# Performance work log

Hardware: AMD Instinct MI355X
Metric: run time of the kernel (lower is better)

## Reference

```python
import jax, jax.numpy as jnp
import numpy as np

B, S, D, H, F, R = 4, 128, 512, 8, 2048, 8
DH = D // H
THRESH = 0.1  # hardcoded in the torch module


def _ln(x, g, b):
    m = x.mean(-1, keepdims=True)
    v = ((x - m) ** 2).mean(-1, keepdims=True)
    return (x - m) * jax.lax.rsqrt(v + 1e-5) * g + b


def setup_inputs() -> dict:
    key = jax.random.key(0)
    ks = jax.random.split(key, 12)
    w = lambda k, shape, std: jax.random.normal(k, shape, jnp.float32) * std
    s = 1.0 / np.sqrt(D)
    qk_std = 2.0 / np.sqrt(D)  # peaky attention so adjacency threshold fires
    return {
        "x": jax.random.normal(ks[0], (B, S, D), jnp.float32),
        "ln1_g": jnp.ones(D, jnp.float32), "ln1_b": jnp.zeros(D, jnp.float32),
        "wq": w(ks[1], (D, D), qk_std), "bq": jnp.zeros(D, jnp.float32),
        "wk": w(ks[2], (D, D), qk_std), "bk": jnp.zeros(D, jnp.float32),
        "wv": w(ks[3], (D, D), s), "bv": jnp.zeros(D, jnp.float32),
        "wo": w(ks[4], (D, D), s), "bo": jnp.zeros(D, jnp.float32),
        "w1": w(ks[5], (D, F), s), "b1": jnp.zeros(F, jnp.float32),
        "w2": w(ks[6], (F, D), 1.0 / np.sqrt(F)), "b2": jnp.zeros(D, jnp.float32),
        "rc_w1": w(ks[7], (2 * D, D), 1.0 / np.sqrt(2 * D)), "rc_b1": jnp.zeros(D, jnp.float32),
        "rc_w2": w(ks[8], (D, R), s), "rc_b2": jnp.zeros(R, jnp.float32),
        "kg_w": w(ks[9], (R, D, D), s),
        "s2n_w": w(ks[10], (D, D), s), "s2n_b": jnp.zeros(D, jnp.float32),
        "ln2_g": jnp.ones(D, jnp.float32), "ln2_b": jnp.zeros(D, jnp.float32),
    }


def reference(x, ln1_g, ln1_b, wq, bq, wk, bk, wv, bv, wo, bo,
              w1, b1, w2, b2, rc_w1, rc_b1, rc_w2, rc_b2,
              kg_w, s2n_w, s2n_b, ln2_g, ln2_b):
    # pre-norm attention
    xn = _ln(x, ln1_g, ln1_b)
    q = (xn @ wq + bq).reshape(B, S, H, DH)
    k = (xn @ wk + bk).reshape(B, S, H, DH)
    v = (xn @ wv + bv).reshape(B, S, H, DH)
    scores = jnp.einsum('bihd,bjhd->bhij', q, k) / np.sqrt(DH)
    attn = jax.nn.softmax(scores, axis=-1)                  # [B,H,S,S]
    ctx = jnp.einsum('bhij,bjhd->bihd', attn, v).reshape(B, S, D)
    attn_out = ctx @ wo + bo
    # FFN -> neural_understanding (no residual, as in source)
    nu = jax.nn.relu(attn_out @ w1 + b1) @ w2 + b2          # [B,S,D]
    # dynamic edge extraction, expressed as a dense mask (jit-safe)
    am = attn.mean(axis=1)                                  # [B,S,S]
    adj = (am > THRESH) & (~jnp.eye(S, dtype=bool))         # u != v
    # relation classifier on every (u,v) pair; mask selects real edges
    a_part = nu @ rc_w1[:D]                                 # concept1 half
    b_part = nu @ rc_w1[D:]                                 # concept2 half
    h = jax.nn.relu(a_part[:, :, None, :] + b_part[:, None, :, :] + rc_b1)  # [B,S,S,D]
    logits = h @ rc_w2 + rc_b2                              # [B,S,S,R]
    pred = jnp.argmax(logits, axis=-1)
    valid = adj & (pred != 0)                               # relation 0 == NONE
    oh = jax.nn.one_hot(pred, R, dtype=nu.dtype) * valid[..., None].astype(nu.dtype)
    # RGCN-style knowledge graph conv: message u -> v with per-relation weight
    transformed = jnp.einsum('bud,rde->bure', nu, kg_w)     # [B,S,R,D]
    agg = jnp.einsum('buvr,bure->bve', oh, transformed)     # [B,S,D]
    reasoned = nu + agg
    neural_result = reasoned @ s2n_w + s2n_b
    out = _ln(x + neural_result, ln2_g, ln2_b)
    return out
```

## Files before the change

kernel.cpp:

```cpp
#include <hip/hip_runtime.h>
#include <hip/hip_bf16.h>

#define B_ 4
#define S_ 128
#define D_ 512
#define H_ 8
#define DH_ 64
#define F_ 2048
#define R_ 8
#define BS_ (B_ * S_)
#define BSD_ (BS_ * D_)
#define E_ 262144

typedef __attribute__((ext_vector_type(8))) short short8;
typedef __attribute__((ext_vector_type(4))) float f32x4;
typedef __attribute__((ext_vector_type(4))) unsigned short ushort4v;

__device__ __forceinline__ void split2(float a, unsigned short& h, unsigned short& l) {
    unsigned u = __float_as_uint(a);
    unsigned hr = (u + 0x7FFFu + ((u >> 16) & 1u)) >> 16;
    h = (unsigned short)hr;
    float lo = a - __uint_as_float(hr << 16);
    unsigned u2 = __float_as_uint(lo);
    l = (unsigned short)((u2 + 0x7FFFu + ((u2 >> 16) & 1u)) >> 16);
}

struct TDesc { const float* s; unsigned short* h; unsigned short* l; int K; int N; int off; };
struct TPack { TDesc d[10]; };

__global__ void prep_kernel(TPack p, int nt, const float* __restrict__ x,
                            const float* __restrict__ g, const float* __restrict__ be,
                            unsigned short* __restrict__ xh, unsigned short* __restrict__ xl) {
    __shared__ float tr[32][33];
    __shared__ float red[256];
    int bid = blockIdx.x;
    if (bid < nt) {
        int wi = 0;
#pragma unroll
        for (int i = 1; i < 10; ++i) if (bid >= p.d[i].off) wi = i;
        const TDesc dd = p.d[wi];
        int t = bid - dd.off;
        int ntk = dd.K / 32;
        int tk = t % ntk, tn = t / ntk;
        int k0 = tk * 32, n0 = tn * 32;
        int col = threadIdx.x & 31, rg = threadIdx.x >> 5;
#pragma unroll
        for (int i = 0; i < 4; ++i) {
            int row = rg * 4 + i;
            tr[row][col] = dd.s[(size_t)(k0 + row) * dd.N + n0 + col];
        }
        __syncthreads();
#pragma unroll
        for (int i = 0; i < 4; ++i) {
            int n = n0 + rg * 4 + i;
            int k = k0 + col;
            unsigned short h, l;
            split2(tr[col][rg * 4 + i], h, l);
            dd.h[(size_t)n * dd.K + k] = h;
            dd.l[(size_t)n * dd.K + k] = l;
        }
    } else {
        int row = bid - nt;
        int t = threadIdx.x;
        const float* xr = x + (size_t)row * D_;
        float v0 = xr[t], v1 = xr[t + 256];
        red[t] = v0 + v1;
        __syncthreads();
        for (int off = 128; off > 0; off >>= 1) { if (t < off) red[t] += red[t + off]; __syncthreads(); }
        float mean = red[0] * (1.0f / D_);
        __syncthreads();
        float d0 = v0 - mean, d1 = v1 - mean;
        red[t] = d0 * d0 + d1 * d1;
        __syncthreads();
        for (int off = 128; off > 0; off >>= 1) { if (t < off) red[t] += red[t + off]; __syncthreads(); }
        float rs = rsqrtf(red[0] * (1.0f / D_) + 1e-5f);
        float o0 = d0 * rs * g[t] + be[t];
        float o1 = d1 * rs * g[t + 256] + be[t + 256];
        unsigned short h, l;
        split2(o0, h, l); xh[(size_t)row * D_ + t] = h;       xl[(size_t)row * D_ + t] = l;
        split2(o1, h, l); xh[(size_t)row * D_ + t + 256] = h; xl[(size_t)row * D_ + t + 256] = l;
    }
}

struct GemmLds {
    unsigned short A[3][2][64][64];
    unsigned short B[3][2][64][64];
};

__device__ __forceinline__ void gload16(const unsigned short* g, unsigned short* l) {
    __builtin_amdgcn_global_load_lds(
        (const __attribute__((address_space(1))) void*)g,
        (__attribute__((address_space(3))) void*)l, 16, 0, 0);
}

__device__ __forceinline__ void vmwait_batches(int nb) {
    if (nb == 2)      asm volatile("s_waitcnt vmcnt(16)" ::: "memory");
    else if (nb == 1) asm volatile("s_waitcnt vmcnt(8)" ::: "memory");
    else              asm volatile("s_waitcnt vmcnt(0)" ::: "memory");
}

__device__ __forceinline__ void mgemm_core(const unsigned short* __restrict__ Ath,
                                           const unsigned short* __restrict__ Atl,
                                           const unsigned short* __restrict__ Bth,
                                           const unsigned short* __restrict__ Btl,
                                           int K, int rowBase, int colBase,
                                           int kStart, int nsteps,
                                           f32x4 acc[2][2], GemmLds* L) {
    int tid = threadIdx.x;
    int w = tid >> 6, lane = tid & 63;
    int lm = lane & 15, quad = lane >> 4;
    int wm = (w & 1) * 32, wn = (w >> 1) * 32;
    int r0 = w * 8 + (lane >> 3);
    int lc = ((lane & 7) ^ (lane >> 3)) * 8;
    int wb = w * 512;
    size_t a0 = (size_t)(rowBase + r0) * K + kStart + lc;
    size_t a1 = (size_t)(rowBase + r0 + 32) * K + kStart + lc;
    size_t b0 = (size_t)(colBase + r0) * K + kStart + lc;
    size_t b1 = (size_t)(colBase + r0 + 32) * K + kStart + lc;
    unsigned short* AB = &L->A[0][0][0][0];
    unsigned short* BB = &L->B[0][0][0][0];
    auto stage = [&](int buf, size_t koff) {
        gload16(&Ath[a0 + koff], AB + buf * 8192 + wb);
        gload16(&Ath[a1 + koff], AB + buf * 8192 + 2048 + wb);
        gload16(&Atl[a0 + koff], AB + buf * 8192 + 4096 + wb);
        gload16(&Atl[a1 + koff], AB + buf * 8192 + 6144 + wb);
        gload16(&Bth[b0 + koff], BB + buf * 8192 + wb);
        gload16(&Bth[b1 + koff], BB + buf * 8192 + 2048 + wb);
        gload16(&Btl[b0 + koff], BB + buf * 8192 + 4096 + wb);
        gload16(&Btl[b1 + koff], BB + buf * 8192 + 6144 + wb);
    };
    stage(0, 0);
    if (nsteps > 1) stage(1, 64);
    if (nsteps > 2) stage(2, 128);
    int b = 0;
    for (int s = 0; s < nsteps; ++s) {
        int last = nsteps - 1;
        int inflight = (s + 2 <= last) ? 2 : (s + 1 <= last) ? 1 : 0;
        vmwait_batches(inflight);
        __builtin_amdgcn_s_barrier();
        __builtin_amdgcn_sched_barrier(0);
#pragma unroll
        for (int sub = 0; sub < 2; ++sub) {
            short8 ah[2], al[2], bh[2], bl[2];
            int pc = ((sub * 4 + quad) ^ (lm & 7)) * 8;
#pragma unroll
            for (int t = 0; t < 2; ++t) {
                int ra = (wm + t * 16 + lm) * 64 + pc;
                int rb = (wn + t * 16 + lm) * 64 + pc;
                ah[t] = *(const short8*)(AB + b * 8192 + ra);
                al[t] = *(const short8*)(AB + b * 8192 + 4096 + ra);
                bh[t] = *(const short8*)(BB + b * 8192 + rb);
                bl[t] = *(const short8*)(BB + b * 8192 + 4096 + rb);
            }
#pragma unroll
            for (int tm = 0; tm < 2; ++tm)
#pragma unroll
                for (int tn = 0; tn < 2; ++tn) {
                    acc[tm][tn] = __builtin_amdgcn_mfma_f32_16x16x32_bf16(ah[tm], bh[tn], acc[tm][tn], 0, 0, 0);
                    acc[tm][tn] = __builtin_amdgcn_mfma_f32_16x16x32_bf16(ah[tm], bl[tn], acc[tm][tn], 0, 0, 0);
                    acc[tm][tn] = __builtin_amdgcn_mfma_f32_16x16x32_bf16(al[tm], bh[tn], acc[tm][tn], 0, 0, 0);
                }
        }
        __builtin_amdgcn_sched_barrier(0);
        __builtin_amdgcn_s_barrier();
        if (s + 3 < nsteps) stage(b, (size_t)(s + 3) * 64);
        b = (b == 2) ? 0 : b + 1;
    }
}

__device__ __forceinline__ void gemm_epilogue(f32x4 acc[2][2], const float* bias,
                                              float* Cf, unsigned short* Ch, unsigned short* Cl,
                                              int N, int relu, int rowBase, int colBase) {
    int tid = threadIdx.x;
    int w = tid >> 6, lane = tid & 63;
    int lm = lane & 15, quad = lane >> 4;
    int wm = (w & 1) * 32, wn = (w >> 1) * 32;
#pragma unroll
    for (int tm = 0; tm < 2; ++tm)
#pragma unroll
        for (int tn = 0; tn < 2; ++tn) {
            int col = colBase + wn + tn * 16 + lm;
            float bi = bias ? bias[col] : 0.f;
#pragma unroll
            for (int r = 0; r < 4; ++r) {
                int row = rowBase + wm + tm * 16 + quad * 4 + r;
                float v = acc[tm][tn][r] + bi;
                if (relu) v = fmaxf(v, 0.f);
                size_t o = (size_t)row * N + col;
                if (Cf) Cf[o] = v;
                if (Ch) {
                    unsigned short sh, sl;
                    split2(v, sh, sl);
                    Ch[o] = sh; Cl[o] = sl;
                }
            }
        }
}

__global__ __launch_bounds__(256) void mgemm_kernel(const unsigned short* __restrict__ Ath,
                                                    const unsigned short* __restrict__ Atl,
                                                    const unsigned short* __restrict__ Bth,
                                                    const unsigned short* __restrict__ Btl,
                                                    const float* __restrict__ bias,
                                                    float* __restrict__ Cf,
                                                    unsigned short* __restrict__ Ch,
                                                    unsigned short* __restrict__ Cl,
                                                    int N, int K, int relu) {
    __shared__ GemmLds L;
    int rowBase = blockIdx.y * 64, colBase = blockIdx.x * 64;
    f32x4 acc[2][2] = {};
    mgemm_core(Ath, Atl, Bth, Btl, K, rowBase, colBase, 0, K / 64, acc, &L);
    gemm_epilogue(acc, bias, Cf, Ch, Cl, N, relu, rowBase, colBase);
}

__global__ __launch_bounds__(256) void mgemm_zw_kernel(const unsigned short* __restrict__ Ath,
                                                       const unsigned short* __restrict__ Atl,
                                                       const unsigned short* __restrict__ Bth,
                                                       const unsigned short* __restrict__ Btl,
                                                       const float* __restrict__ b0,
                                                       const float* __restrict__ b1,
                                                       const float* __restrict__ b2,
                                                       float* __restrict__ Cbase,
                                                       int M, int N, int K) {
    __shared__ GemmLds L;
    int z = blockIdx.z;
    const unsigned short* bth = Bth + (size_t)z * K * N;
    const unsigned short* btl = Btl + (size_t)z * K * N;
    const float* bias = (z == 0) ? b0 : (z == 1) ? b1 : b2;
    float* C = Cbase + (size_t)z * M * N;
    int rowBase = blockIdx.y * 64, colBase = blockIdx.x * 64;
    f32x4 acc[2][2] = {};
    mgemm_core(Ath, Atl, bth, btl, K, rowBase, colBase, 0, K / 64, acc, &L);
    gemm_epilogue(acc, bias, C, nullptr, nullptr, N, 0, rowBase, colBase);
}

__global__ __launch_bounds__(256) void mgemm_part_kernel(const unsigned short* __restrict__ Ath,
                                                         const unsigned short* __restrict__ Atl,
                                                         const unsigned short* __restrict__ Bth,
                                                         const unsigned short* __restrict__ Btl,
                                                         float* __restrict__ Cbase,
                                                         int M, int N, int K) {
    __shared__ GemmLds L;
    int ks = gridDim.z, z = blockIdx.z;
    int kLen = K / ks, kStart = z * kLen;
    float* C = Cbase + (size_t)z * M * N;
    int rowBase = blockIdx.y * 64, colBase = blockIdx.x * 64;
    f32x4 acc[2][2] = {};
    mgemm_core(Ath, Atl, Bth, Btl, K, rowBase, colBase, kStart, kLen / 64, acc, &L);
    gemm_epilogue(acc, nullptr, C, nullptr, nullptr, N, 0, rowBase, colBase);
}

__global__ __launch_bounds__(256) void wo_adj_kernel(const unsigned short* __restrict__ Ath,
                                                     const unsigned short* __restrict__ Atl,
                                                     const unsigned short* __restrict__ Bth,
                                                     const unsigned short* __restrict__ Btl,
                                                     const float* __restrict__ bias,
                                                     unsigned short* __restrict__ Ch,
                                                     unsigned short* __restrict__ Cl,
                                                     const float* __restrict__ attnP,
                                                     unsigned long long* __restrict__ adjm) {
    __shared__ GemmLds L;
    int bid = blockIdx.x;
    if (bid < 64) {
        int rowBase = (bid >> 3) * 64, colBase = (bid & 7) * 64;
        f32x4 acc[2][2] = {};
        mgemm_core(Ath, Atl, Bth, Btl, D_, rowBase, colBase, 0, D_ / 64, acc, &L);
        gemm_epilogue(acc, bias, nullptr, Ch, Cl, D_, 0, rowBase, colBase);
    } else {
        int idx = (bid - 64) * 256 + threadIdx.x;
        int j = idx & (S_ - 1);
        int bi = idx >> 7;
        int i = bi & (S_ - 1);
        int b = bi >> 7;
        float s = 0.f;
#pragma unroll
        for (int h = 0; h < H_; ++h) s += attnP[(((size_t)(b * H_ + h)) * S_ + i) * S_ + j];
        s *= (1.0f / H_);
        int pred = (s > 0.1f && i != j) ? 1 : 0;
        unsigned long long m = __ballot(pred);
        if ((threadIdx.x & 63) == 0)
            adjm[(size_t)bi * 2 + ((threadIdx.x >> 6) & 1)] = m;
    }
}

__global__ void reduce4_kernel(const float* __restrict__ part, const float* __restrict__ b2,
                               float* __restrict__ nu,
                               unsigned short* __restrict__ nh, unsigned short* __restrict__ nl) {
    int base = blockIdx.x * 1024 + threadIdx.x * 4;
    f32x4 s = *(const f32x4*)&b2[base & (D_ - 1)];
#pragma unroll
    for (int z = 0; z < 4; ++z) s += *(const f32x4*)&part[(size_t)z * BSD_ + base];
    *(f32x4*)&nu[base] = s;
    ushort4v hv, lv;
#pragma unroll
    for (int i = 0; i < 4; ++i) { unsigned short h, l; split2(s[i], h, l); hv[i] = h; lv[i] = l; }
    *(ushort4v*)&nh[base] = hv;
    *(ushort4v*)&nl[base] = lv;
}

__global__ void reduce8_kernel(const float* __restrict__ part, const float* __restrict__ nu,
                               unsigned short* __restrict__ rh, unsigned short* __restrict__ rl) {
    int base = blockIdx.x * 1024 + threadIdx.x * 4;
    f32x4 s = *(const f32x4*)&nu[base];
#pragma unroll
    for (int z = 0; z < 8; ++z) s += *(const f32x4*)&part[(size_t)z * BSD_ + base];
    ushort4v hv, lv;
#pragma unroll
    for (int i = 0; i < 4; ++i) { unsigned short h, l; split2(s[i], h, l); hv[i] = h; lv[i] = l; }
    *(ushort4v*)&rh[base] = hv;
    *(ushort4v*)&rl[base] = lv;
}

__global__ __launch_bounds__(512) void attn_kernel2(const float* __restrict__ q,
                                                    const float* __restrict__ k,
                                                    const float* __restrict__ v,
                                                    float* __restrict__ attnP,
                                                    unsigned short* __restrict__ ch,
                                                    unsigned short* __restrict__ cl) {
    __shared__ float ksm[S_][DH_ + 3];
    __shared__ float qsm[16][DH_];
    __shared__ float psm[16][S_];
    int tid = threadIdx.x;
    int w = tid >> 6, lane = tid & 63;
    int blk = blockIdx.x;
    int ig = blk & 7;
    int bh = blk >> 3;
    int h = bh & (H_ - 1);
    int b = bh >> 3;
    int i0 = ig * 16;
    const float* kb = k + (size_t)b * S_ * D_ + h * DH_;
    for (int j = w; j < S_; j += 8) ksm[j][lane] = kb[(size_t)j * D_ + lane];
    for (int il = w; il < 16; il += 8)
        qsm[il][lane] = q[(size_t)(b * S_ + i0 + il) * D_ + h * DH_ + lane];
    __syncthreads();
    const float* vb = v + (size_t)b * S_ * D_ + h * DH_ + lane;
#pragma unroll
    for (int c = 0; c < 2; ++c) {
        int il = w + c * 8;
        int i = i0 + il;
        float s0 = 0.f, s1 = 0.f;
#pragma unroll 8
        for (int d = 0; d < DH_; ++d) {
            float qd = qsm[il][d];
            s0 += qd * ksm[lane][d];
            s1 += qd * ksm[lane + 64][d];
        }
        s0 *= 0.125f; s1 *= 0.125f;
        float m = fmaxf(s0, s1);
#pragma unroll
        for (int off = 32; off > 0; off >>= 1) m = fmaxf(m, __shfl_xor(m, off));
        float e0 = __expf(s0 - m), e1 = __expf(s1 - m);
        float sum = e0 + e1;
#pragma unroll
        for (int off = 32; off > 0; off >>= 1) sum += __shfl_xor(sum, off);
        float inv = 1.f / sum;
        float p0 = e0 * inv, p1 = e1 * inv;
        float* arow = attnP + ((size_t)(b * H_ + h) * S_ + i) * S_;
        arow[lane] = p0;
        arow[lane + 64] = p1;
        psm[il][lane] = p0;
        psm[il][lane + 64] = p1;
        float acc = 0.f;
        for (int j = 0; j < S_; ++j) acc += psm[il][j] * vb[(size_t)j * D_];
        unsigned short sh, sl;
        split2(acc, sh, sl);
        size_t o = (size_t)(b * S_ + i) * D_ + h * DH_ + lane;
        ch[o] = sh; cl[o] = sl;
    }
}

__global__ __launch_bounds__(512) void mbuild_edge_kernel(const float* __restrict__ nu,
                                                          const float* __restrict__ a_part,
                                                          const float* __restrict__ b_part,
                                                          const float* __restrict__ rc_b1,
                                                          const float* __restrict__ rc_w2,
                                                          const float* __restrict__ rc_b2,
                                                          const unsigned long long* __restrict__ adjm,
                                                          unsigned short* __restrict__ Mh,
                                                          unsigned short* __restrict__ Ml) {
    __shared__ float acc[R_ * D_];
    __shared__ float w2t[R_][D_];
    __shared__ float bsm[D_];
    __shared__ int rl[S_];
    int blk = blockIdx.x;
    int vv = blk & (S_ - 1);
    int b = blk >> 7;
    int t = threadIdx.x;
    int w = t >> 6, lane = t & 63;
    for (int i = t; i < R_ * D_; i += 512) {
        w2t[i & 7][i >> 3] = rc_w2[i];
        acc[i] = 0.f;
    }
    bsm[t] = b_part[(size_t)blk * D_ + t];
    __syncthreads();
    int wsel = vv >> 6, bsh = vv & 63;
    for (int u = w; u < S_; u += 8) {
        unsigned long long word = adjm[((size_t)(b * S_ + u)) * 2 + wsel];
        if ((word >> bsh) & 1ull) {
            const float* ap = a_part + (size_t)(b * S_ + u) * D_;
            float lp[R_];
#pragma unroll
            for (int r = 0; r < R_; ++r) lp[r] = 0.f;
#pragma unroll
            for (int jj = 0; jj < D_ / 64; ++jj) {
                int d = lane + jj * 64;
                float hv = fmaxf(ap[d] + bsm[d] + rc_b1[d], 0.f);
#pragma unroll
                for (int r = 0; r < R_; ++r) lp[r] += hv * w2t[r][d];
            }
#pragma unroll
            for (int r = 0; r < R_; ++r) {
#pragma unroll
                for (int off = 32; off > 0; off >>= 1) lp[r] += __shfl_down(lp[r], off);
            }
            if (lane == 0) {
                float best = lp[0] + rc_b2[0];
                int bi = 0;
#pragma unroll
                for (int r = 1; r < R_; ++r) {
                    float L = lp[r] + rc_b2[r];
                    if (L > best) { best = L; bi = r; }
                }
                rl[u] = bi;
            }
        } else if (lane == 0) {
            rl[u] = 0;
        }
    }
    __syncthreads();
    for (int u = 0; u < S_; ++u) {
        int r = rl[u];
        if (r > 0) acc[r * D_ + t] += nu[(size_t)(b * S_ + u) * D_ + t];
    }
    __syncthreads();
    unsigned short* Hrow = Mh + (size_t)blk * (R_ * D_);
    unsigned short* Lrow = Ml + (size_t)blk * (R_ * D_);
    for (int i = t; i < R_ * D_; i += 512) {
        unsigned short sh, sl;
        split2(acc[i], sh, sl);
        Hrow[i] = sh; Lrow[i] = sl;
    }
}

__global__ void ln2_kernel(const float* __restrict__ x, const float* __restrict__ y,
                           const float* __restrict__ g, const float* __restrict__ be,
                           float* __restrict__ out) {
    int row = blockIdx.x;
    int t = threadIdx.x;
    __shared__ float red[256];
    float v0 = x[row * D_ + t]       + y[row * D_ + t];
    float v1 = x[row * D_ + t + 256] + y[row * D_ + t + 256];
    red[t] = v0 + v1;
    __syncthreads();
    for (int off = 128; off > 0; off >>= 1) {
        if (t < off) red[t] += red[t + off];
        __syncthreads();
    }
    float mean = red[0] * (1.0f / D_);
    __syncthreads();
    float d0 = v0 - mean, d1 = v1 - mean;
    red[t] = d0 * d0 + d1 * d1;
    __syncthreads();
    for (int off = 128; off > 0; off >>= 1) {
        if (t < off) red[t] += red[t + off];
        __syncthreads();
    }
    float rs = rsqrtf(red[0] * (1.0f / D_) + 1e-5f);
    out[row * D_ + t]       = d0 * rs * g[t]       + be[t];
    out[row * D_ + t + 256] = d1 * rs * g[t + 256] + be[t + 256];
}

extern "C" void kernel_launch(void* const* d_in, const int* in_sizes, int n_in,
                              void* d_out, int out_size, void* d_ws, size_t ws_size,
                              hipStream_t stream) {
    const float* x     = (const float*)d_in[0];
    const float* ln1_g = (const float*)d_in[1];
    const float* ln1_b = (const float*)d_in[2];
    const float* wq    = (const float*)d_in[3];
    const float* bq    = (const float*)d_in[4];
    const float* wk    = (const float*)d_in[5];
    const float* bk    = (const float*)d_in[6];
    const float* wv    = (const float*)d_in[7];
    const float* bv    = (const float*)d_in[8];
    const float* wo    = (const float*)d_in[9];
    const float* bo    = (const float*)d_in[10];
    const float* w1    = (const float*)d_in[11];
    const float* b1    = (const float*)d_in[12];
    const float* w2    = (const float*)d_in[13];
    const float* b2    = (const float*)d_in[14];
    const float* rc_w1 = (const float*)d_in[15];
    const float* rc_b1 = (const float*)d_in[16];
    const float* rc_w2 = (const float*)d_in[17];
    const float* rc_b2 = (const float*)d_in[18];
    const float* kg_w  = (const float*)d_in[19];
    const float* s2n_w = (const float*)d_in[20];
    const float* s2n_b = (const float*)d_in[21];
    const float* ln2_g = (const float*)d_in[22];
    const float* ln2_b = (const float*)d_in[23];
    float* out = (float*)d_out;

    const int BS  = BS_;
    const int BSD = BSD_;

    unsigned short* wt = (unsigned short*)d_ws;
    unsigned short* qkv_h = wt;
    unsigned short* qkv_l = wt + 3 * E_;
    unsigned short* wo_h  = wt + 6 * E_;
    unsigned short* wo_l  = wt + 7 * E_;
    unsigned short* w1_h  = wt + 8 * E_;
    unsigned short* w1_l  = wt + 12 * E_;
    unsigned short* w2_h  = wt + 16 * E_;
    unsigned short* w2_l  = wt + 20 * E_;
    unsigned short* rc_h  = wt + 24 * E_;
    unsigned short* rc_l  = wt + 26 * E_;
    unsigned short* kg_h  = wt + 28 * E_;
    unsigned short* kg_l  = wt + 36 * E_;
    unsigned short* s2_h  = wt + 44 * E_;
    unsigned short* s2_l  = wt + 45 * E_;

    unsigned short* xn_h  = wt + 46 * E_;
    unsigned short* xn_l  = xn_h + BSD;
    unsigned short* ctx_h = xn_l + BSD;
    unsigned short* ctx_l = ctx_h + BSD;
    unsigned short* ao_h  = ctx_l + BSD;
    unsigned short* ao_l  = ao_h + BSD;
    unsigned short* hid_h = ao_l + BSD;
    unsigned short* hid_l = hid_h + (size_t)BS * F_;
    unsigned short* nu_h  = hid_l + (size_t)BS * F_;
    unsigned short* nu_l  = nu_h + BSD;
    unsigned short* mb_h  = nu_l + BSD;
    unsigned short* mb_l  = mb_h + (size_t)BS * R_ * D_;
    unsigned short* rs_h  = mb_l + (size_t)BS * R_ * D_;
    unsigned short* rs_l  = rs_h + BSD;

    float* fbase  = (float*)(rs_l + BSD);
    float* q      = fbase;
    float* v_     = q + 2 * BSD;
    float* apart  = q + 3 * BSD;
    float* nu     = apart + 2 * BSD;
    float* y      = nu + BSD;
    float* part4  = y + BSD;
    float* part8  = part4 + 4 * BSD;
    float* attnP  = part8 + 8 * BSD;

    unsigned long long* adjm = (unsigned long long*)(attnP + 2097152);

    TPack tp;
    int off = 0;
    auto setd = [&](int i, const float* s, unsigned short* h, unsigned short* l, int K, int N) {
        tp.d[i] = TDesc{s, h, l, K, N, off};
        off += (K / 32) * (N / 32);
    };
    setd(0, wq, qkv_h,          qkv_l,          D_, D_);
    setd(1, wk, qkv_h + E_,     qkv_l + E_,     D_, D_);
    setd(2, wv, qkv_h + 2 * E_, qkv_l + 2 * E_, D_, D_);
    setd(3, wo, wo_h, wo_l, D_, D_);
    setd(4, w1, w1_h, w1_l, D_, F_);
    setd(5, w2, w2_h, w2_l, F_, D_);
    setd(6, rc_w1,            rc_h,      rc_l,      D_, D_);
    setd(7, rc_w1 + D_ * D_,  rc_h + E_, rc_l + E_, D_, D_);
    setd(8, kg_w, kg_h, kg_l, R_ * D_, D_);
    setd(9, s2n_w, s2_h, s2_l, D_, D_);
    hipLaunchKernelGGL(prep_kernel, dim3(off + BS), dim3(256), 0, stream, tp, off,
                       x, ln1_g, ln1_b, xn_h, xn_l);

    hipLaunchKernelGGL(mgemm_zw_kernel, dim3(D_ / 64, BS / 64, 3), dim3(256), 0, stream,
                       xn_h, xn_l, qkv_h, qkv_l, bq, bk, bv, q, BS, D_, D_);
    hipLaunchKernelGGL(attn_kernel2, dim3(B_ * H_ * 8), dim3(512), 0, stream,
                       q, q + BSD, v_, attnP, ctx_h, ctx_l);
    hipLaunchKernelGGL(wo_adj_kernel, dim3(64 + 256), dim3(256), 0, stream,
                       ctx_h, ctx_l, wo_h, wo_l, bo, ao_h, ao_l, attnP, adjm);
    hipLaunchKernelGGL(mgemm_kernel, dim3(F_ / 64, BS / 64), dim3(256), 0, stream,
                       ao_h, ao_l, w1_h, w1_l, b1, (float*)nullptr, hid_h, hid_l, F_, D_, 1);
    hipLaunchKernelGGL(mgemm_part_kernel, dim3(D_ / 64, BS / 64, 4), dim3(256), 0, stream,
                       hid_h, hid_l, w2_h, w2_l, part4, BS, D_, F_);
    hipLaunchKernelGGL(reduce4_kernel, dim3(BSD / 1024), dim3(256), 0, stream,
                       part4, b2, nu, nu_h, nu_l);
    hipLaunchKernelGGL(mgemm_zw_kernel, dim3(D_ / 64, BS / 64, 2), dim3(256), 0, stream,
                       nu_h, nu_l, rc_h, rc_l, (const float*)nullptr, (const float*)nullptr,
                       (const float*)nullptr, apart, BS, D_, D_);
    hipLaunchKernelGGL(mbuild_edge_kernel, dim3(BS), dim3(512), 0, stream,
                       nu, apart, apart + BSD, rc_b1, rc_w2, rc_b2, adjm, mb_h, mb_l);
    hipLaunchKernelGGL(mgemm_part_kernel, dim3(D_ / 64, BS / 64, 8), dim3(256), 0, stream,
                       mb_h, mb_l, kg_h, kg_l, part8, BS, D_, R_ * D_);
    hipLaunchKernelGGL(reduce8_kernel, dim3(BSD / 1024), dim3(256), 0, stream,
                       part8, nu, rs_h, rs_l);
    hipLaunchKernelGGL(mgemm_kernel, dim3(D_ / 64, BS / 64), dim3(256), 0, stream,
                       rs_h, rs_l, s2_h, s2_l, s2n_b, y, (unsigned short*)nullptr,
                       (unsigned short*)nullptr, D_, D_, 0);
    hipLaunchKernelGGL(ln2_kernel, dim3(BS), dim3(256), 0, stream, x, y, ln2_g, ln2_b, out);
}
```

Baseline: 220.1 us.

## Use single-barrier 3-buffer pipeline in GEMM core and split-K final projection fused with LN

The GEMM main loop now issues the next-but-one tile load right after the top barrier, which drops the second barrier per k-step while keeping a three-buffer ring with a prefetch distance of two. The final s2n projection changes from a 32-block GEMM to a 4-way split-K partial GEMM. The partials, bias and residual are summed inside a new reduce+LayerNorm kernel, so the separate y buffer pass goes away. The aim is more parallelism for the small final GEMM and less barrier overhead in every GEMM. The cost is extra partial-sum traffic and a shallower prefetch depth.

```diff
diff --git a/kernel.cpp b/kernel.cpp
--- a/kernel.cpp
+++ b/kernel.cpp
@@ -91,12 +91,6 @@
     __builtin_amdgcn_global_load_lds(
         (const __attribute__((address_space(1))) void*)g,
         (__attribute__((address_space(3))) void*)l, 16, 0, 0);
-}
-
-__device__ __forceinline__ void vmwait_batches(int nb) {
-    if (nb == 2)      asm volatile("s_waitcnt vmcnt(16)" ::: "memory");
-    else if (nb == 1) asm volatile("s_waitcnt vmcnt(8)" ::: "memory");
-    else              asm volatile("s_waitcnt vmcnt(0)" ::: "memory");
 }
 
 __device__ __forceinline__ void mgemm_core(const unsigned short* __restrict__ Ath,
@@ -131,14 +125,13 @@
     };
     stage(0, 0);
     if (nsteps > 1) stage(1, 64);
-    if (nsteps > 2) stage(2, 128);
-    int b = 0;
     for (int s = 0; s < nsteps; ++s) {
-        int last = nsteps - 1;
-        int inflight = (s + 2 <= last) ? 2 : (s + 1 <= last) ? 1 : 0;
-        vmwait_batches(inflight);
+        int b = s % 3;
+        if (s + 2 <= nsteps) asm volatile("s_waitcnt vmcnt(8)" ::: "memory");
+        else                 asm volatile("s_waitcnt vmcnt(0)" ::: "memory");
         __builtin_amdgcn_s_barrier();
         __builtin_amdgcn_sched_barrier(0);
+        if (s + 2 < nsteps) stage((s + 2) % 3, (size_t)(s + 2) * 64);
 #pragma unroll
         for (int sub = 0; sub < 2; ++sub) {
             short8 ah[2], al[2], bh[2], bl[2];
@@ -162,9 +155,6 @@
                 }
         }
         __builtin_amdgcn_sched_barrier(0);
-        __builtin_amdgcn_s_barrier();
-        if (s + 3 < nsteps) stage(b, (size_t)(s + 3) * 64);
-        b = (b == 2) ? 0 : b + 1;
     }
 }
 
@@ -442,14 +432,20 @@
     }
 }
 
-__global__ void ln2_kernel(const float* __restrict__ x, const float* __restrict__ y,
-                           const float* __restrict__ g, const float* __restrict__ be,
-                           float* __restrict__ out) {
+__global__ void reduceln_kernel(const float* __restrict__ part, const float* __restrict__ x,
+                                const float* __restrict__ sb, const float* __restrict__ g,
+                                const float* __restrict__ be, float* __restrict__ out) {
     int row = blockIdx.x;
     int t = threadIdx.x;
     __shared__ float red[256];
-    float v0 = x[row * D_ + t]       + y[row * D_ + t];
-    float v1 = x[row * D_ + t + 256] + y[row * D_ + t + 256];
+    float y0 = sb[t], y1 = sb[t + 256];
+#pragma unroll
+    for (int z = 0; z < 4; ++z) {
+        y0 += part[(size_t)z * BSD_ + (size_t)row * D_ + t];
+        y1 += part[(size_t)z * BSD_ + (size_t)row * D_ + t + 256];
+    }
+    float v0 = x[(size_t)row * D_ + t]       + y0;
+    float v1 = x[(size_t)row * D_ + t + 256] + y1;
     red[t] = v0 + v1;
     __syncthreads();
     for (int off = 128; off > 0; off >>= 1) {
@@ -466,8 +462,8 @@
         __syncthreads();
     }
     float rs = rsqrtf(red[0] * (1.0f / D_) + 1e-5f);
-    out[row * D_ + t]       = d0 * rs * g[t]       + be[t];
-    out[row * D_ + t + 256] = d1 * rs * g[t + 256] + be[t + 256];
+    out[(size_t)row * D_ + t]       = d0 * rs * g[t]       + be[t];
+    out[(size_t)row * D_ + t + 256] = d1 * rs * g[t + 256] + be[t + 256];
 }
 
 extern "C" void kernel_launch(void* const* d_in, const int* in_sizes, int n_in,
@@ -585,8 +581,8 @@
                        mb_h, mb_l, kg_h, kg_l, part8, BS, D_, R_ * D_);
     hipLaunchKernelGGL(reduce8_kernel, dim3(BSD / 1024), dim3(256), 0, stream,
                        part8, nu, rs_h, rs_l);
-    hipLaunchKernelGGL(mgemm_kernel, dim3(D_ / 64, BS / 64), dim3(256), 0, stream,
-                       rs_h, rs_l, s2_h, s2_l, s2n_b, y, (unsigned short*)nullptr,
-                       (unsigned short*)nullptr, D_, D_, 0);
-    hipLaunchKernelGGL(ln2_kernel, dim3(BS), dim3(256), 0, stream, x, y, ln2_g, ln2_b, out);
-}
+    hipLaunchKernelGGL(mgemm_part_kernel, dim3(D_ / 64, BS / 64, 4), dim3(256), 0, stream,
+                       rs_h, rs_l, s2_h, s2_l, part4, BS, D_, D_);
+    hipLaunchKernelGGL(reduceln_kernel, dim3(BS), dim3(256), 0, stream,
+                       part4, x, s2n_b, ln2_g, ln2_b, out);
+}
```

Result: no change. 216.6 us, median of 2 (-1.6%).
